# Kernel tuning notes

Hardware: AMD Instinct MI355X
Metric: run time of the kernel (lower is better)

The kernel has to match this reference:

```python
import jax, jax.numpy as jnp
import numpy as np
import math

BS, N_CTX, WIDTH, HEADS = 4, 2048, 1024, 16
INIT_SCALE = 0.02

def setup_inputs() -> dict:
    key = jax.random.key(0)
    ks = jax.random.split(key, 5)
    x = jax.random.normal(ks[0], (BS, N_CTX, WIDTH), dtype=jnp.float32)
    w_qkv = jax.random.normal(ks[1], (WIDTH, 3 * WIDTH), dtype=jnp.float32) * INIT_SCALE
    b_qkv = jnp.zeros((3 * WIDTH,), dtype=jnp.float32)
    w_proj = jax.random.normal(ks[2], (WIDTH, WIDTH), dtype=jnp.float32) * INIT_SCALE
    b_proj = jnp.zeros((WIDTH,), dtype=jnp.float32)
    return {"x": x, "w_qkv": w_qkv, "b_qkv": b_qkv, "w_proj": w_proj, "b_proj": b_proj}

def reference(x, w_qkv, b_qkv, w_proj, b_proj):
    bs, n_ctx, width = x.shape
    heads = HEADS
    qkv = x @ w_qkv + b_qkv  # [b, t, 3*width]
    attn_ch = (3 * width) // heads // 3  # head dim
    scale = 1.0 / math.sqrt(math.sqrt(attn_ch))
    qkv = qkv.reshape(bs, n_ctx, heads, 3 * attn_ch)
    q, k, v = jnp.split(qkv, 3, axis=-1)  # each [b, s, h, c]
    weight = jnp.einsum('bthc,bshc->bhts', q * scale, k * scale)
    weight = jax.nn.softmax(weight.astype(jnp.float32), axis=-1).astype(weight.dtype)
    out = jnp.einsum('bhts,bshc->bthc', weight, v).reshape(bs, n_ctx, width)
    return out @ w_proj + b_proj
```

## Files before the change

kernel.cpp:

```cpp
#include <hip/hip_runtime.h>
#include <stdint.h>

#define MM   8192
#define KK   1024
#define NQKV 3072
#define TT   2048
#define HH   16
#define DD   64

typedef __attribute__((ext_vector_type(8))) short bf16x8;
typedef __attribute__((ext_vector_type(4))) short short4v;
typedef __attribute__((ext_vector_type(4))) float f32x4;
typedef __attribute__((ext_vector_type(16))) float f32x16;
typedef __attribute__((ext_vector_type(4))) unsigned int u32x4;

#define MFMA16(a,b,c)  __builtin_amdgcn_mfma_f32_16x16x32_bf16(a,b,c,0,0,0)
#define MFMA32(a,b,c)  __builtin_amdgcn_mfma_f32_32x32x16_bf16(a,b,c,0,0,0)

static __device__ __forceinline__ short f2bf(float f) {
    uint32_t u = __float_as_uint(f);
    uint32_t r = (u + 0x7fffu + ((u >> 16) & 1u)) >> 16;
    return (short)r;
}

static __device__ __forceinline__ uint32_t cvtpk(float a, float b) {
    uint32_t r;
    asm("v_cvt_pk_bf16_f32 %0, %1, %2" : "=v"(r) : "v"(a), "v"(b));
    return r;
}

static __device__ __forceinline__ void plswap(uint32_t& x, uint32_t& y) {
    asm("v_permlane32_swap_b32 %0, %1" : "+v"(x), "+v"(y));
}

static __device__ __forceinline__ float tsum16(const f32x16& p) {
    float a0 = p[0] + p[8],  a1 = p[1] + p[9];
    float a2 = p[2] + p[10], a3 = p[3] + p[11];
    float a4 = p[4] + p[12], a5 = p[5] + p[13];
    float a6 = p[6] + p[14], a7 = p[7] + p[15];
    float b0 = a0 + a4, b1 = a1 + a5, b2 = a2 + a6, b3 = a3 + a7;
    return (b0 + b2) + (b1 + b3);
}

__global__ __launch_bounds__(256) void convert_x(const float* __restrict__ x,
                                                 short* __restrict__ xb, int n) {
    int i = (blockIdx.x * 256 + threadIdx.x) * 4;
    if (i >= n) return;
    float4 v = *(const float4*)(x + i);
    short4v o;
    o[0] = f2bf(v.x); o[1] = f2bf(v.y); o[2] = f2bf(v.z); o[3] = f2bf(v.w);
    *(short4v*)(xb + i) = o;
}

__global__ __launch_bounds__(256) void transpose_w(const float* __restrict__ Wf,
                                                   short* __restrict__ Wt, int K, int N) {
    __shared__ float tile[32][33];
    const int n0 = blockIdx.x * 32, k0 = blockIdx.y * 32;
    const int tx = threadIdx.x & 31, ty = threadIdx.x >> 5;
#pragma unroll
    for (int i = 0; i < 4; ++i) {
        int k = ty + i * 8;
        tile[k][tx] = Wf[(size_t)(k0 + k) * N + n0 + tx];
    }
    __syncthreads();
#pragma unroll
    for (int i = 0; i < 4; ++i) {
        int n = ty + i * 8;
        Wt[(size_t)(n0 + n) * K + k0 + tx] = f2bf(tile[tx][n]);
    }
}

template <int N, bool F32OUT>
__global__ __launch_bounds__(256) void gemm_bt(const short* __restrict__ A,
                                               const short* __restrict__ Bt,
                                               const float* __restrict__ bias,
                                               void* __restrict__ Cout, int K) {
    __shared__ short As[128 * 72];
    __shared__ short Bs[128 * 72];
    const int tid = threadIdx.x, lane = tid & 63, wave = tid >> 6;
    const int l15 = lane & 15, lg = lane >> 4;
    const int wm = wave >> 1, wn = wave & 1;
    const int m0 = blockIdx.y * 128, n0 = blockIdx.x * 128;

    f32x4 zero = {0.f, 0.f, 0.f, 0.f};
    f32x4 acc[4][4];
#pragma unroll
    for (int i = 0; i < 4; ++i)
#pragma unroll
        for (int j = 0; j < 4; ++j) acc[i][j] = zero;

    const int sr = tid >> 3, sc = (tid & 7) * 8;

    for (int kt = 0; kt < K; kt += 64) {
#pragma unroll
        for (int p = 0; p < 4; ++p) {
            int row = sr + p * 32;
            *(bf16x8*)(&As[row * 72 + sc]) = *(const bf16x8*)(A + (size_t)(m0 + row) * K + kt + sc);
            *(bf16x8*)(&Bs[row * 72 + sc]) = *(const bf16x8*)(Bt + (size_t)(n0 + row) * K + kt + sc);
        }
        __syncthreads();
#pragma unroll
        for (int ks = 0; ks < 2; ++ks) {
            bf16x8 af[4], bfr[4];
#pragma unroll
            for (int i = 0; i < 4; ++i)
                af[i] = *(const bf16x8*)(&As[(wm * 64 + i * 16 + l15) * 72 + ks * 32 + lg * 8]);
#pragma unroll
            for (int j = 0; j < 4; ++j)
                bfr[j] = *(const bf16x8*)(&Bs[(wn * 64 + j * 16 + l15) * 72 + ks * 32 + lg * 8]);
#pragma unroll
            for (int i = 0; i < 4; ++i)
#pragma unroll
                for (int j = 0; j < 4; ++j)
                    acc[i][j] = MFMA16(af[i], bfr[j], acc[i][j]);
        }
        __syncthreads();
    }
#pragma unroll
    for (int j = 0; j < 4; ++j) {
        int col = n0 + wn * 64 + j * 16 + l15;
        float bv = bias[col];
#pragma unroll
        for (int i = 0; i < 4; ++i) {
            int row = m0 + wm * 64 + i * 16 + lg * 4;
#pragma unroll
            for (int r = 0; r < 4; ++r) {
                float v = acc[i][j][r] + bv;
                if (F32OUT)
                    ((float*)Cout)[(size_t)(row + r) * N + col] = v;
                else
                    ((short*)Cout)[(size_t)(row + r) * N + col] = f2bf(v);
            }
        }
    }
}

__global__ __launch_bounds__(256) void repack_kv(const short* __restrict__ QKV,
                                                 short* __restrict__ Kf,
                                                 short* __restrict__ Vf) {
    __shared__ short Kl[64 * 72];
    __shared__ short Vl[64 * 72];
    const int t = blockIdx.x, bh = blockIdx.y;
    const int b = bh >> 4, h = bh & 15;
    const int tid = threadIdx.x;
    const int r = tid >> 3, c = (tid & 7) * 8;
    const short* kvbase = QKV + (size_t)(b * TT + t * 64) * NQKV + h * 192;
#pragma unroll
    for (int p = 0; p < 2; ++p) {
        int row = r + p * 32;
        *(bf16x8*)(&Kl[row * 72 + c]) = *(const bf16x8*)(kvbase + (size_t)row * NQKV + 64 + c);
        *(bf16x8*)(&Vl[row * 72 + c]) = *(const bf16x8*)(kvbase + (size_t)row * NQKV + 128 + c);
    }
    __syncthreads();
    short* kfb = Kf + ((size_t)bh * 32 + t) * 4096;
    short* vfb = Vf + ((size_t)bh * 32 + t) * 4096;
#pragma unroll
    for (int p = 0; p < 2; ++p) {
        int q = tid + p * 256;
        int lane = q & 63, dc = (q >> 6) & 3, half = q >> 8;
        int l31 = lane & 31, hi = lane >> 5;
        bf16x8 kv = *(const bf16x8*)(&Kl[(half * 32 + l31) * 72 + hi * 8 + dc * 16]);
        *(bf16x8*)(kfb + q * 8) = kv;
        bf16x8 vv;
#pragma unroll
        for (int j = 0; j < 8; ++j)
            vv[j] = Vl[(hi * 8 + dc * 16 + j) * 72 + half * 32 + l31];
        *(bf16x8*)(vfb + q * 8) = vv;
    }
}

static __device__ __forceinline__ void attn_tile(
    const bf16x8 (&kc0)[4], const bf16x8 (&kc1)[4],
    bf16x8 (&kn0)[4], bf16x8 (&kn1)[4],
    const bf16x8 (&qf)[4],
    const short* __restrict__ kfb, const short* __restrict__ vfb,
    int t, int lane8,
    f32x16& o0, f32x16& o1, float& ls) {

    int nxt = t + 1; nxt = (nxt < TT / 64) ? nxt : 0;
    const short* np = kfb + (size_t)nxt * 4096 + lane8;
#pragma unroll
    for (int dc = 0; dc < 4; ++dc) kn0[dc] = *(const bf16x8*)(np + dc * 512);
#pragma unroll
    for (int dc = 0; dc < 4; ++dc) kn1[dc] = *(const bf16x8*)(np + 2048 + dc * 512);

    const short* vp = vfb + (size_t)t * 4096 + lane8;
    bf16x8 vf0[4], vf1[4];
#pragma unroll
    for (int ks = 0; ks < 4; ++ks) vf0[ks] = *(const bf16x8*)(vp + ks * 512);
#pragma unroll
    for (int ks = 0; ks < 4; ++ks) vf1[ks] = *(const bf16x8*)(vp + 2048 + ks * 512);

    f32x16 s0, s1;
#pragma unroll
    for (int i = 0; i < 16; ++i) { s0[i] = 0.f; s1[i] = 0.f; }
#pragma unroll
    for (int dc = 0; dc < 4; ++dc) s0 = MFMA32(kc0[dc], qf[dc], s0);
#pragma unroll
    for (int dc = 0; dc < 4; ++dc) s1 = MFMA32(kc1[dc], qf[dc], s1);

#pragma unroll
    for (int i = 0; i < 16; ++i) s0[i] = exp2f(s0[i]);
#pragma unroll
    for (int i = 0; i < 16; ++i) s1[i] = exp2f(s1[i]);

    float rs = tsum16(s0) + tsum16(s1);
    rs += __shfl_xor(rs, 32);
    ls += rs;

    uint32_t a0 = cvtpk(s0[0], s0[1]),   a1 = cvtpk(s0[2], s0[3]);
    uint32_t b0 = cvtpk(s0[4], s0[5]),   b1 = cvtpk(s0[6], s0[7]);
    plswap(a0, b0); plswap(a1, b1);
    uint32_t c0 = cvtpk(s0[8], s0[9]),   c1 = cvtpk(s0[10], s0[11]);
    uint32_t d0 = cvtpk(s0[12], s0[13]), d1 = cvtpk(s0[14], s0[15]);
    plswap(c0, d0); plswap(c1, d1);
    uint32_t e0 = cvtpk(s1[0], s1[1]),   e1 = cvtpk(s1[2], s1[3]);
    uint32_t f0 = cvtpk(s1[4], s1[5]),   f1 = cvtpk(s1[6], s1[7]);
    plswap(e0, f0); plswap(e1, f1);
    uint32_t g0 = cvtpk(s1[8], s1[9]),   g1 = cvtpk(s1[10], s1[11]);
    uint32_t h0 = cvtpk(s1[12], s1[13]), h1 = cvtpk(s1[14], s1[15]);
    plswap(g0, h0); plswap(g1, h1);
    u32x4 w0 = {a0, a1, b0, b1};
    u32x4 w1 = {c0, c1, d0, d1};
    u32x4 w2 = {e0, e1, f0, f1};
    u32x4 w3 = {g0, g1, h0, h1};
    bf16x8 pa0 = __builtin_bit_cast(bf16x8, w0);
    bf16x8 pa1 = __builtin_bit_cast(bf16x8, w1);
    bf16x8 pa2 = __builtin_bit_cast(bf16x8, w2);
    bf16x8 pa3 = __builtin_bit_cast(bf16x8, w3);

    o0 = MFMA32(vf0[0], pa0, o0);
    o0 = MFMA32(vf0[1], pa1, o0);
    o0 = MFMA32(vf0[2], pa2, o0);
    o0 = MFMA32(vf0[3], pa3, o0);
    o1 = MFMA32(vf1[0], pa0, o1);
    o1 = MFMA32(vf1[1], pa1, o1);
    o1 = MFMA32(vf1[2], pa2, o1);
    o1 = MFMA32(vf1[3], pa3, o1);
}

__global__ __launch_bounds__(128) void attn_fwd(const short* __restrict__ QKV,
                                                const short* __restrict__ Kf,
                                                const short* __restrict__ Vf,
                                                short* __restrict__ Out) {
    const int qb = blockIdx.x, bh = blockIdx.y;
    const int b = bh >> 4, h = bh & 15;
    const int lane = threadIdx.x & 63, wave = threadIdx.x >> 6;
    const int l31 = lane & 31, hi = lane >> 5;
    const int q0 = qb * 64 + wave * 32;
    const int lane8 = lane * 8;

    const short* qptr = QKV + (size_t)(b * TT + q0 + l31) * NQKV + h * 192 + hi * 8;
    bf16x8 qf[4];
#pragma unroll
    for (int dc = 0; dc < 4; ++dc) qf[dc] = *(const bf16x8*)(qptr + dc * 16);

    const float cc = 0.18033688011112042f;
    {
        short* qs = (short*)qf;
#pragma unroll
        for (int i = 0; i < 32; ++i) {
            float v = __uint_as_float(((uint32_t)(uint16_t)qs[i]) << 16) * cc;
            qs[i] = f2bf(v);
        }
    }

    const short* kfb = Kf + (size_t)bh * 32 * 4096;
    const short* vfb = Vf + (size_t)bh * 32 * 4096;

    f32x16 o0, o1;
#pragma unroll
    for (int i = 0; i < 16; ++i) { o0[i] = 0.f; o1[i] = 0.f; }
    float ls = 0.f;

    bf16x8 kA0[4], kA1[4], kB0[4], kB1[4];
#pragma unroll
    for (int dc = 0; dc < 4; ++dc) kA0[dc] = *(const bf16x8*)(kfb + dc * 512 + lane8);
#pragma unroll
    for (int dc = 0; dc < 4; ++dc) kA1[dc] = *(const bf16x8*)(kfb + 2048 + dc * 512 + lane8);

    for (int t = 0; t < TT / 64; t += 2) {
        attn_tile(kA0, kA1, kB0, kB1, qf, kfb, vfb, t,     lane8, o0, o1, ls);
        attn_tile(kB0, kB1, kA0, kA1, qf, kfb, vfb, t + 1, lane8, o0, o1, ls);
    }

    float inv = 1.0f / ls;
    short* orow = Out + (size_t)(b * TT + q0 + l31) * (HH * DD) + h * DD;
#pragma unroll
    for (int g = 0; g < 4; ++g) {
        short4v v0, v1;
#pragma unroll
        for (int r = 0; r < 4; ++r) {
            v0[r] = f2bf(o0[g * 4 + r] * inv);
            v1[r] = f2bf(o1[g * 4 + r] * inv);
        }
        *(short4v*)(orow + g * 8 + hi * 4) = v0;
        *(short4v*)(orow + 32 + g * 8 + hi * 4) = v1;
    }
}

extern "C" void kernel_launch(void* const* d_in, const int* in_sizes, int n_in,
                              void* d_out, int out_size, void* d_ws, size_t ws_size,
                              hipStream_t stream) {
    const float* x      = (const float*)d_in[0];
    const float* w_qkv  = (const float*)d_in[1];
    const float* b_qkv  = (const float*)d_in[2];
    const float* w_proj = (const float*)d_in[3];
    const float* b_proj = (const float*)d_in[4];
    float* out = (float*)d_out;

    char* ws = (char*)d_ws;
    short* xb     = (short*)(ws);
    short* wqkvt  = (short*)(ws + 16777216);
    short* wprojt = (short*)(ws + 23068672);
    short* qkv    = (short*)(ws + 25165824);
    short* kf     = (short*)(ws + 75497472);
    short* vf     = (short*)(ws);
    short* ao     = (short*)(ws + 92274688);

    convert_x<<<8192, 256, 0, stream>>>(x, xb, MM * KK);
    transpose_w<<<dim3(NQKV / 32, KK / 32), 256, 0, stream>>>(w_qkv, wqkvt, KK, NQKV);
    transpose_w<<<dim3(KK / 32, KK / 32), 256, 0, stream>>>(w_proj, wprojt, KK, KK);
    gemm_bt<NQKV, false><<<dim3(NQKV / 128, MM / 128), 256, 0, stream>>>(xb, wqkvt, b_qkv, qkv, KK);
    repack_kv<<<dim3(TT / 64, 64), 256, 0, stream>>>(qkv, kf, vf);
    attn_fwd<<<dim3(TT / 64, 64), 128, 0, stream>>>(qkv, kf, vf, ao);
    gemm_bt<KK, true><<<dim3(KK / 128, MM / 128), 256, 0, stream>>>(ao, wprojt, b_proj, out, KK);
}
```

Measured before the change: 225.5 us.

## Stage V tiles in double-buffered LDS via async global-to-LDS loads, widen attention blocks

The attention kernel now uses 4 waves per block covering 128 queries. V tiles are shared across those waves through a double-buffered LDS buffer, filled with global_load_lds for the next tile while the current one is consumed. Each wave previously read V straight from global memory, so this cuts redundant V traffic. exp2f is replaced by the raw v_exp_f32 instruction. The cost is a block-wide barrier on every tile, and the softmax still has no max subtraction, so it depends on the scores staying small.

```diff
diff --git a/kernel.cpp b/kernel.cpp
--- a/kernel.cpp
+++ b/kernel.cpp
@@ -17,10 +17,21 @@
 #define MFMA16(a,b,c)  __builtin_amdgcn_mfma_f32_16x16x32_bf16(a,b,c,0,0,0)
 #define MFMA32(a,b,c)  __builtin_amdgcn_mfma_f32_32x32x16_bf16(a,b,c,0,0,0)
 
+#define GLOAD_LDS16(g, l)                                                      \
+    __builtin_amdgcn_global_load_lds(                                          \
+        (const __attribute__((address_space(1))) void*)(g),                    \
+        (__attribute__((address_space(3))) void*)(l), 16, 0, 0)
+
 static __device__ __forceinline__ short f2bf(float f) {
     uint32_t u = __float_as_uint(f);
     uint32_t r = (u + 0x7fffu + ((u >> 16) & 1u)) >> 16;
     return (short)r;
+}
+
+static __device__ __forceinline__ float fexp2(float x) {
+    float r;
+    asm("v_exp_f32 %0, %1" : "=v"(r) : "v"(x));
+    return r;
 }
 
 static __device__ __forceinline__ uint32_t cvtpk(float a, float b) {
@@ -174,8 +185,15 @@
     bf16x8 (&kn0)[4], bf16x8 (&kn1)[4],
     const bf16x8 (&qf)[4],
     const short* __restrict__ kfb, const short* __restrict__ vfb,
-    int t, int lane8,
+    const short* vlds_cur, short* vlds_nxt,
+    int t, int wave, int lane8,
     f32x16& o0, f32x16& o1, float& ls) {
+
+    bf16x8 vf0[4], vf1[4];
+#pragma unroll
+    for (int ks = 0; ks < 4; ++ks) vf0[ks] = *(const bf16x8*)(vlds_cur + ks * 512 + lane8);
+#pragma unroll
+    for (int ks = 0; ks < 4; ++ks) vf1[ks] = *(const bf16x8*)(vlds_cur + 2048 + ks * 512 + lane8);
 
     int nxt = t + 1; nxt = (nxt < TT / 64) ? nxt : 0;
     const short* np = kfb + (size_t)nxt * 4096 + lane8;
@@ -183,13 +201,9 @@
     for (int dc = 0; dc < 4; ++dc) kn0[dc] = *(const bf16x8*)(np + dc * 512);
 #pragma unroll
     for (int dc = 0; dc < 4; ++dc) kn1[dc] = *(const bf16x8*)(np + 2048 + dc * 512);
-
-    const short* vp = vfb + (size_t)t * 4096 + lane8;
-    bf16x8 vf0[4], vf1[4];
-#pragma unroll
-    for (int ks = 0; ks < 4; ++ks) vf0[ks] = *(const bf16x8*)(vp + ks * 512);
-#pragma unroll
-    for (int ks = 0; ks < 4; ++ks) vf1[ks] = *(const bf16x8*)(vp + 2048 + ks * 512);
+    const short* vsrc = vfb + (size_t)nxt * 4096 + wave * 1024 + lane8;
+    GLOAD_LDS16(vsrc,       vlds_nxt + wave * 1024);
+    GLOAD_LDS16(vsrc + 512, vlds_nxt + wave * 1024 + 512);
 
     f32x16 s0, s1;
 #pragma unroll
@@ -200,9 +214,9 @@
     for (int dc = 0; dc < 4; ++dc) s1 = MFMA32(kc1[dc], qf[dc], s1);
 
 #pragma unroll
-    for (int i = 0; i < 16; ++i) s0[i] = exp2f(s0[i]);
-#pragma unroll
-    for (int i = 0; i < 16; ++i) s1[i] = exp2f(s1[i]);
+    for (int i = 0; i < 16; ++i) s0[i] = fexp2(s0[i]);
+#pragma unroll
+    for (int i = 0; i < 16; ++i) s1[i] = fexp2(s1[i]);
 
     float rs = tsum16(s0) + tsum16(s1);
     rs += __shfl_xor(rs, 32);
@@ -237,17 +251,20 @@
     o1 = MFMA32(vf1[1], pa1, o1);
     o1 = MFMA32(vf1[2], pa2, o1);
     o1 = MFMA32(vf1[3], pa3, o1);
-}
-
-__global__ __launch_bounds__(128) void attn_fwd(const short* __restrict__ QKV,
+
+    __syncthreads();
+}
+
+__global__ __launch_bounds__(256) void attn_fwd(const short* __restrict__ QKV,
                                                 const short* __restrict__ Kf,
                                                 const short* __restrict__ Vf,
                                                 short* __restrict__ Out) {
+    __shared__ short Vlds[2][4096];
     const int qb = blockIdx.x, bh = blockIdx.y;
     const int b = bh >> 4, h = bh & 15;
     const int lane = threadIdx.x & 63, wave = threadIdx.x >> 6;
     const int l31 = lane & 31, hi = lane >> 5;
-    const int q0 = qb * 64 + wave * 32;
+    const int q0 = qb * 128 + wave * 32;
     const int lane8 = lane * 8;
 
     const short* qptr = QKV + (size_t)(b * TT + q0 + l31) * NQKV + h * 192 + hi * 8;
@@ -273,15 +290,23 @@
     for (int i = 0; i < 16; ++i) { o0[i] = 0.f; o1[i] = 0.f; }
     float ls = 0.f;
 
+    {
+        const short* vsrc = vfb + wave * 1024 + lane8;
+        GLOAD_LDS16(vsrc,       &Vlds[0][wave * 1024]);
+        GLOAD_LDS16(vsrc + 512, &Vlds[0][wave * 1024 + 512]);
+    }
     bf16x8 kA0[4], kA1[4], kB0[4], kB1[4];
 #pragma unroll
     for (int dc = 0; dc < 4; ++dc) kA0[dc] = *(const bf16x8*)(kfb + dc * 512 + lane8);
 #pragma unroll
     for (int dc = 0; dc < 4; ++dc) kA1[dc] = *(const bf16x8*)(kfb + 2048 + dc * 512 + lane8);
+    __syncthreads();
 
     for (int t = 0; t < TT / 64; t += 2) {
-        attn_tile(kA0, kA1, kB0, kB1, qf, kfb, vfb, t,     lane8, o0, o1, ls);
-        attn_tile(kB0, kB1, kA0, kA1, qf, kfb, vfb, t + 1, lane8, o0, o1, ls);
+        attn_tile(kA0, kA1, kB0, kB1, qf, kfb, vfb, &Vlds[0][0], &Vlds[1][0],
+                  t,     wave, lane8, o0, o1, ls);
+        attn_tile(kB0, kB1, kA0, kA1, qf, kfb, vfb, &Vlds[1][0], &Vlds[0][0],
+                  t + 1, wave, lane8, o0, o1, ls);
     }
 
     float inv = 1.0f / ls;
@@ -323,6 +348,6 @@
     transpose_w<<<dim3(KK / 32, KK / 32), 256, 0, stream>>>(w_proj, wprojt, KK, KK);
     gemm_bt<NQKV, false><<<dim3(NQKV / 128, MM / 128), 256, 0, stream>>>(xb, wqkvt, b_qkv, qkv, KK);
     repack_kv<<<dim3(TT / 64, 64), 256, 0, stream>>>(qkv, kf, vf);
-    attn_fwd<<<dim3(TT / 64, 64), 128, 0, stream>>>(qkv, kf, vf, ao);
+    attn_fwd<<<dim3(TT / 128, 64), 256, 0, stream>>>(qkv, kf, vf, ao);
     gemm_bt<KK, true><<<dim3(KK / 128, MM / 128), 256, 0, stream>>>(ao, wprojt, b_proj, out, KK);
 }
```

Measured after the change: 217.5 us. -3.6%, faster.

## Fuse fp32-to-bf16 conversion into QKV GEMM and retune attention kernel

Applied to the files above, without the earlier changes.

Drops the separate convert_x pass by loading fp32 activations directly in the QKV GEMM and packing them to bf16 with v_cvt_pk_bf16_f32 before storing to shared memory. This removes a full write and reread of the converted input. The attention inner loop uses raw v_exp_f32 instead of exp2f and raises wave priority around MFMA groups. Attention blocks grow to four waves covering 128 queries. The GEMM A loads now fetch twice the bytes per tile, and the rounding mode of the conversion may differ slightly from the software round-to-nearest-even.

```diff
diff --git a/kernel.cpp b/kernel.cpp
--- a/kernel.cpp
+++ b/kernel.cpp
@@ -21,6 +21,12 @@
     uint32_t u = __float_as_uint(f);
     uint32_t r = (u + 0x7fffu + ((u >> 16) & 1u)) >> 16;
     return (short)r;
+}
+
+static __device__ __forceinline__ float fexp2(float x) {
+    float r;
+    asm("v_exp_f32 %0, %1" : "=v"(r) : "v"(x));
+    return r;
 }
 
 static __device__ __forceinline__ uint32_t cvtpk(float a, float b) {
@@ -42,16 +48,6 @@
     return (b0 + b2) + (b1 + b3);
 }
 
-__global__ __launch_bounds__(256) void convert_x(const float* __restrict__ x,
-                                                 short* __restrict__ xb, int n) {
-    int i = (blockIdx.x * 256 + threadIdx.x) * 4;
-    if (i >= n) return;
-    float4 v = *(const float4*)(x + i);
-    short4v o;
-    o[0] = f2bf(v.x); o[1] = f2bf(v.y); o[2] = f2bf(v.z); o[3] = f2bf(v.w);
-    *(short4v*)(xb + i) = o;
-}
-
 __global__ __launch_bounds__(256) void transpose_w(const float* __restrict__ Wf,
                                                    short* __restrict__ Wt, int K, int N) {
     __shared__ float tile[32][33];
@@ -70,8 +66,8 @@
     }
 }
 
-template <int N, bool F32OUT>
-__global__ __launch_bounds__(256) void gemm_bt(const short* __restrict__ A,
+template <int N, bool F32OUT, bool F32A>
+__global__ __launch_bounds__(256) void gemm_bt(const void* __restrict__ Ain,
                                                const short* __restrict__ Bt,
                                                const float* __restrict__ bias,
                                                void* __restrict__ Cout, int K) {
@@ -95,7 +91,17 @@
 #pragma unroll
         for (int p = 0; p < 4; ++p) {
             int row = sr + p * 32;
-            *(bf16x8*)(&As[row * 72 + sc]) = *(const bf16x8*)(A + (size_t)(m0 + row) * K + kt + sc);
+            if (F32A) {
+                const float* Af = (const float*)Ain;
+                float4 lo = *(const float4*)(Af + (size_t)(m0 + row) * K + kt + sc);
+                float4 hi = *(const float4*)(Af + (size_t)(m0 + row) * K + kt + sc + 4);
+                u32x4 pk = {cvtpk(lo.x, lo.y), cvtpk(lo.z, lo.w),
+                            cvtpk(hi.x, hi.y), cvtpk(hi.z, hi.w)};
+                *(bf16x8*)(&As[row * 72 + sc]) = __builtin_bit_cast(bf16x8, pk);
+            } else {
+                const short* Ab = (const short*)Ain;
+                *(bf16x8*)(&As[row * 72 + sc]) = *(const bf16x8*)(Ab + (size_t)(m0 + row) * K + kt + sc);
+            }
             *(bf16x8*)(&Bs[row * 72 + sc]) = *(const bf16x8*)(Bt + (size_t)(n0 + row) * K + kt + sc);
         }
         __syncthreads();
@@ -194,15 +200,17 @@
     f32x16 s0, s1;
 #pragma unroll
     for (int i = 0; i < 16; ++i) { s0[i] = 0.f; s1[i] = 0.f; }
+    __builtin_amdgcn_s_setprio(1);
 #pragma unroll
     for (int dc = 0; dc < 4; ++dc) s0 = MFMA32(kc0[dc], qf[dc], s0);
 #pragma unroll
     for (int dc = 0; dc < 4; ++dc) s1 = MFMA32(kc1[dc], qf[dc], s1);
-
-#pragma unroll
-    for (int i = 0; i < 16; ++i) s0[i] = exp2f(s0[i]);
-#pragma unroll
-    for (int i = 0; i < 16; ++i) s1[i] = exp2f(s1[i]);
+    __builtin_amdgcn_s_setprio(0);
+
+#pragma unroll
+    for (int i = 0; i < 16; ++i) s0[i] = fexp2(s0[i]);
+#pragma unroll
+    for (int i = 0; i < 16; ++i) s1[i] = fexp2(s1[i]);
 
     float rs = tsum16(s0) + tsum16(s1);
     rs += __shfl_xor(rs, 32);
@@ -229,6 +237,7 @@
     bf16x8 pa2 = __builtin_bit_cast(bf16x8, w2);
     bf16x8 pa3 = __builtin_bit_cast(bf16x8, w3);
 
+    __builtin_amdgcn_s_setprio(1);
     o0 = MFMA32(vf0[0], pa0, o0);
     o0 = MFMA32(vf0[1], pa1, o0);
     o0 = MFMA32(vf0[2], pa2, o0);
@@ -237,9 +246,10 @@
     o1 = MFMA32(vf1[1], pa1, o1);
     o1 = MFMA32(vf1[2], pa2, o1);
     o1 = MFMA32(vf1[3], pa3, o1);
-}
-
-__global__ __launch_bounds__(128) void attn_fwd(const short* __restrict__ QKV,
+    __builtin_amdgcn_s_setprio(0);
+}
+
+__global__ __launch_bounds__(256) void attn_fwd(const short* __restrict__ QKV,
                                                 const short* __restrict__ Kf,
                                                 const short* __restrict__ Vf,
                                                 short* __restrict__ Out) {
@@ -247,7 +257,7 @@
     const int b = bh >> 4, h = bh & 15;
     const int lane = threadIdx.x & 63, wave = threadIdx.x >> 6;
     const int l31 = lane & 31, hi = lane >> 5;
-    const int q0 = qb * 64 + wave * 32;
+    const int q0 = qb * 128 + wave * 32;
     const int lane8 = lane * 8;
 
     const short* qptr = QKV + (size_t)(b * TT + q0 + l31) * NQKV + h * 192 + hi * 8;
@@ -310,19 +320,17 @@
     float* out = (float*)d_out;
 
     char* ws = (char*)d_ws;
-    short* xb     = (short*)(ws);
+    short* vf     = (short*)(ws);
     short* wqkvt  = (short*)(ws + 16777216);
     short* wprojt = (short*)(ws + 23068672);
     short* qkv    = (short*)(ws + 25165824);
     short* kf     = (short*)(ws + 75497472);
-    short* vf     = (short*)(ws);
     short* ao     = (short*)(ws + 92274688);
 
-    convert_x<<<8192, 256, 0, stream>>>(x, xb, MM * KK);
     transpose_w<<<dim3(NQKV / 32, KK / 32), 256, 0, stream>>>(w_qkv, wqkvt, KK, NQKV);
     transpose_w<<<dim3(KK / 32, KK / 32), 256, 0, stream>>>(w_proj, wprojt, KK, KK);
-    gemm_bt<NQKV, false><<<dim3(NQKV / 128, MM / 128), 256, 0, stream>>>(xb, wqkvt, b_qkv, qkv, KK);
+    gemm_bt<NQKV, false, true><<<dim3(NQKV / 128, MM / 128), 256, 0, stream>>>(x, wqkvt, b_qkv, qkv, KK);
     repack_kv<<<dim3(TT / 64, 64), 256, 0, stream>>>(qkv, kf, vf);
-    attn_fwd<<<dim3(TT / 64, 64), 128, 0, stream>>>(qkv, kf, vf, ao);
-    gemm_bt<KK, true><<<dim3(KK / 128, MM / 128), 256, 0, stream>>>(ao, wprojt, b_proj, out, KK);
-}
+    attn_fwd<<<dim3(TT / 128, 64), 256, 0, stream>>>(qkv, kf, vf, ao);
+    gemm_bt<KK, true, false><<<dim3(KK / 128, MM / 128), 256, 0, stream>>>(ao, wprojt, b_proj, out, KK);
+}
```

Result: no change. 223.6 us (-0.8%).
